# Optimization experiments

Hardware: AMD Instinct MI355X
Metric: run time of the kernel (lower is better)

Reference implementation:

```python
import jax, jax.numpy as jnp
import numpy as np

D = 1024
HS = 64
NH = D // HS


def setup_inputs() -> dict:
    key = jax.random.key(0)
    ks = jax.random.split(key, 8)
    B, S = 2, 2048
    x = jax.random.normal(ks[0], (B, S, D), dtype=jnp.float32)
    y = jax.random.normal(ks[1], (B, S, D), dtype=jnp.float32)
    pad_mask = jax.random.randint(ks[2], (B, S), 0, 2).astype(jnp.int32)
    sc = 1.0 / np.sqrt(D)
    Wq = jax.random.normal(ks[3], (D, D), dtype=jnp.float32) * sc
    Wk = jax.random.normal(ks[4], (D, D), dtype=jnp.float32) * sc
    Wv = jax.random.normal(ks[5], (D, D), dtype=jnp.float32) * sc
    Wp = jax.random.normal(ks[6], (D, D), dtype=jnp.float32) * sc
    bp = jnp.zeros((D,), dtype=jnp.float32)
    return {"x": x, "y": y, "pad_mask": pad_mask, "Wq": Wq, "Wk": Wk, "Wv": Wv, "Wp": Wp, "bp": bp}


def reference(x, y, pad_mask, Wq, Wk, Wv, Wp, bp):
    B, S, _ = x.shape
    # torch Linear: out = in @ W.T  (bias=False for q/k/v)
    q = (y @ Wq.T).reshape(B, S, NH, HS).transpose(0, 2, 1, 3)  # [B,H,S,hs]
    k = (x @ Wk.T).reshape(B, S, NH, HS).transpose(0, 2, 1, 3)
    v = (x @ Wv.T).reshape(B, S, NH, HS).transpose(0, 2, 1, 3)
    att = jnp.einsum('bhqd,bhkd->bhqk', q, k) * (HS ** -0.5)  # [B,H,S,S]
    att = jnp.where((pad_mask == 0)[:, None, None, :], -jnp.inf, att)
    att = jax.nn.softmax(att, axis=-1)
    out = jnp.einsum('bhqk,bhkd->bhqd', att, v)  # [B,H,S,hs]
    out = out.transpose(0, 2, 1, 3).reshape(B, S, D)
    return out @ Wp.T + bp
```

## Files before the change

### kernel.cpp

```cpp
#include <hip/hip_runtime.h>
#include <hip/hip_bf16.h>
#include <stdint.h>

typedef unsigned short u16;
typedef unsigned int u32;
typedef float __attribute__((ext_vector_type(4))) f32x4;
typedef __bf16 __attribute__((ext_vector_type(8))) bfrag;
typedef u16 __attribute__((ext_vector_type(8))) u16x8;

#define DEV static __device__ __forceinline__

DEV u16 f2bf(float f) {
  union { float f; u32 u; } c; c.f = f;
  u32 u = c.u;
  u += 0x7fffu + ((u >> 16) & 1u);
  return (u16)(u >> 16);
}

DEV u16 bf16bits(float f) {
  __hip_bfloat16 h = __float2bfloat16(f);
  return *reinterpret_cast<u16*>(&h);
}

typedef const u32 __attribute__((address_space(1)))* gas_t;
typedef u32 __attribute__((address_space(3)))* las_t;

DEV void async16(const void* g, void* l) {
  __builtin_amdgcn_global_load_lds((gas_t)(uintptr_t)g, (las_t)(uintptr_t)l, 16, 0, 0);
}

__global__ __launch_bounds__(256) void convert_all(
    const float* __restrict__ x, const float* __restrict__ y,
    const float* __restrict__ wq, const float* __restrict__ wk,
    const float* __restrict__ wv, const float* __restrict__ wp,
    u16* __restrict__ xb, u16* __restrict__ yb,
    u16* __restrict__ wqb, u16* __restrict__ wkb,
    u16* __restrict__ wvb, u16* __restrict__ wpb) {
  const int NX4 = (2 * 2048 * 1024) / 4;
  const int NW4 = (1024 * 1024) / 4;
  const int total = 2 * NX4 + 4 * NW4;
  for (int i = blockIdx.x * blockDim.x + threadIdx.x; i < total;
       i += gridDim.x * blockDim.x) {
    const float4* s; ushort4* d; int off;
    if (i < NX4) { s = (const float4*)x; d = (ushort4*)xb; off = i; }
    else if (i < 2 * NX4) { s = (const float4*)y; d = (ushort4*)yb; off = i - NX4; }
    else {
      int k = i - 2 * NX4; int wsel = k >> 18; off = k & (NW4 - 1);
      s = (const float4*)(wsel == 0 ? wq : wsel == 1 ? wk : wsel == 2 ? wv : wp);
      d = (ushort4*)(wsel == 0 ? wqb : wsel == 1 ? wkb : wsel == 2 ? wvb : wpb);
    }
    float4 v = s[off];
    ushort4 o; o.x = f2bf(v.x); o.y = f2bf(v.y); o.z = f2bf(v.z); o.w = f2bf(v.w);
    d[off] = o;
  }
}

__global__ __launch_bounds__(256, 3) void gemm_qkv(
    const u16* __restrict__ xb, const u16* __restrict__ yb,
    const u16* __restrict__ wqb, const u16* __restrict__ wkb,
    const u16* __restrict__ wvb,
    u16* __restrict__ Qb, u16* __restrict__ Kb2, u16* __restrict__ Vtb) {
  const int Kd = 1024, Nd = 1024;
  __shared__ __align__(16) u16 Als[128 * 32];
  __shared__ __align__(16) u16 Bls[128 * 32];
  __shared__ __align__(16) u16 Tls[4][64 * 72];

  const int gid = blockIdx.x;
  const int seg = gid >> 8;
  const int bb = gid & 255;
  const int m0 = (bb >> 3) * 128, n0 = (bb & 7) * 128;
  const u16* A  = (seg == 0) ? yb : xb;
  const u16* Bw = (seg == 0) ? wqb : (seg == 1 ? wkb : wvb);

  const int t = threadIdx.x;
  const int lane = t & 63, w = t >> 6;
  const int wr = w >> 1, wc = w & 1;
  const int r15 = lane & 15, g = lane >> 4;
  const int rs = t >> 2, sg = t & 3;

  f32x4 acc[4][4] = {{}};
  const u16* ga = A + (size_t)(m0 + rs) * Kd + sg * 8;
  const u16* gb = Bw + (size_t)(n0 + rs) * Kd + sg * 8;

  for (int k0 = 0; k0 < Kd; k0 += 32) {
    async16(ga + k0, &Als[t * 8]);
    async16(ga + 64 * Kd + k0, &Als[(t + 256) * 8]);
    async16(gb + k0, &Bls[t * 8]);
    async16(gb + 64 * Kd + k0, &Bls[(t + 256) * 8]);
    __syncthreads();
    bfrag af[4], bfr[4];
#pragma unroll
    for (int i = 0; i < 4; i++)
      af[i] = *(const bfrag*)&Als[(wr * 64 + i * 16 + r15) * 32 + g * 8];
#pragma unroll
    for (int i = 0; i < 4; i++)
      bfr[i] = *(const bfrag*)&Bls[(wc * 64 + i * 16 + r15) * 32 + g * 8];
#pragma unroll
    for (int i = 0; i < 4; i++)
#pragma unroll
      for (int j = 0; j < 4; j++)
        acc[i][j] = __builtin_amdgcn_mfma_f32_16x16x32_bf16(af[i], bfr[j], acc[i][j], 0, 0, 0);
    __syncthreads();
  }

  if (seg < 2) {
    u16* C = (seg == 0) ? Qb : Kb2;
    const float scale = (seg == 0) ? 0.125f : 1.0f;
#pragma unroll
    for (int i = 0; i < 4; i++) {
#pragma unroll
      for (int j = 0; j < 4; j++) {
        int col = n0 + wc * 64 + j * 16 + r15;
        int row = m0 + wr * 64 + i * 16 + g * 4;
#pragma unroll
        for (int r = 0; r < 4; r++)
          C[(size_t)(row + r) * Nd + col] = f2bf(acc[i][j][r] * scale);
      }
    }
  } else {
#pragma unroll
    for (int i = 0; i < 4; i++)
#pragma unroll
      for (int j = 0; j < 4; j++)
#pragma unroll
        for (int r = 0; r < 4; r++)
          Tls[w][(j * 16 + r15) * 72 + (i * 16 + g * 4 + r)] = f2bf(acc[i][j][r]);
#pragma unroll
    for (int it = 0; it < 8; ++it) {
      int slot = lane + it * 64;
      int nl = slot >> 3, sgm = slot & 7;
      int4 vrow = *(const int4*)&Tls[w][nl * 72 + sgm * 8];
      int col = n0 + wc * 64 + nl;
      int h = col >> 6, hs = col & 63;
      int rowg = m0 + wr * 64 + sgm * 8;
      int b = rowg >> 11, s = rowg & 2047;
      *(int4*)&Vtb[(((size_t)b * 16 + h) * 64 + hs) * 2048 + s] = vrow;
    }
  }
}

__global__ __launch_bounds__(256, 3) void gemm_proj(
    const u16* __restrict__ A, const u16* __restrict__ Bw,
    float* __restrict__ C, const float* __restrict__ bias) {
  const int Kd = 1024, Nd = 1024;
  __shared__ __align__(16) u16 Als[128 * 32];
  __shared__ __align__(16) u16 Bls[128 * 32];
  const int t = threadIdx.x;
  const int lane = t & 63, w = t >> 6;
  const int wr = w >> 1, wc = w & 1;
  const int r15 = lane & 15, g = lane >> 4;
  const int m0 = blockIdx.y * 128, n0 = blockIdx.x * 128;
  const int rs = t >> 2, sg = t & 3;

  f32x4 acc[4][4] = {{}};
  const u16* ga = A + (size_t)(m0 + rs) * Kd + sg * 8;
  const u16* gb = Bw + (size_t)(n0 + rs) * Kd + sg * 8;

  for (int k0 = 0; k0 < Kd; k0 += 32) {
    async16(ga + k0, &Als[t * 8]);
    async16(ga + 64 * Kd + k0, &Als[(t + 256) * 8]);
    async16(gb + k0, &Bls[t * 8]);
    async16(gb + 64 * Kd + k0, &Bls[(t + 256) * 8]);
    __syncthreads();
    bfrag af[4], bfr[4];
#pragma unroll
    for (int i = 0; i < 4; i++)
      af[i] = *(const bfrag*)&Als[(wr * 64 + i * 16 + r15) * 32 + g * 8];
#pragma unroll
    for (int i = 0; i < 4; i++)
      bfr[i] = *(const bfrag*)&Bls[(wc * 64 + i * 16 + r15) * 32 + g * 8];
#pragma unroll
    for (int i = 0; i < 4; i++)
#pragma unroll
      for (int j = 0; j < 4; j++)
        acc[i][j] = __builtin_amdgcn_mfma_f32_16x16x32_bf16(af[i], bfr[j], acc[i][j], 0, 0, 0);
    __syncthreads();
  }

#pragma unroll
  for (int i = 0; i < 4; i++) {
#pragma unroll
    for (int j = 0; j < 4; j++) {
      int col = n0 + wc * 64 + j * 16 + r15;
      int row = m0 + wr * 64 + i * 16 + g * 4;
      float bv = bias[col];
#pragma unroll
      for (int r = 0; r < 4; r++)
        C[(size_t)(row + r) * Nd + col] = acc[i][j][r] + bv;
    }
  }
}

__global__ __launch_bounds__(256, 2) void attn_fwd(
    const u16* __restrict__ Q, const u16* __restrict__ Kb,
    const u16* __restrict__ Vt, const int* __restrict__ mask,
    u16* __restrict__ O) {
  __shared__ __align__(16) u16 Kls[64 * 64];
  __shared__ __align__(16) u16 Vls[64 * 64];
  __shared__ __align__(16) u16 Pls[4][32 * 64];
  __shared__ float biasl[64];

  const int bid = blockIdx.x;
  const int swz = (bid & 7) * 64 + (bid >> 3);
  const int qblk = swz & 15, bh = swz >> 4;
  const int b = bh >> 4, h = bh & 15;
  const int t = threadIdx.x, lane = t & 63, w = t >> 6;
  const int r15 = lane & 15, g = lane >> 4;
  const int qbase = qblk * 128 + w * 32;

  bfrag aQ[2][2];
  {
    const u16* Qg = Q + ((size_t)b * 2048 + qbase) * 1024 + h * 64;
#pragma unroll
    for (int mf = 0; mf < 2; ++mf)
#pragma unroll
      for (int ks = 0; ks < 2; ++ks)
        aQ[mf][ks] = *(const bfrag*)&Qg[(size_t)(mf * 16 + r15) * 1024 + ks * 32 + g * 8];
  }

  bfrag ones;
  {
    u16x8 ob = {0x3F80, 0x3F80, 0x3F80, 0x3F80, 0x3F80, 0x3F80, 0x3F80, 0x3F80};
    ones = *(bfrag*)&ob;
  }

  f32x4 oacc[2][4] = {};
  f32x4 osum[2] = {};

  const u16* Kg = Kb + (size_t)b * 2048 * 1024 + h * 64;
  const u16* Vg = Vt + (size_t)bh * 64 * 2048;
  const int* mg = mask + b * 2048;

  const int kr = t >> 2, kc = (t & 3) * 16;
  const int swr = (kr & 7) << 3;
  const int rdx = (r15 & 7) << 3;
  int4 nk0, nk1, nv0, nv1; float nbias = 0.f;

  auto stage_load = [&](int kv0) {
    nk0 = *(const int4*)&Kg[(size_t)(kv0 + kr) * 1024 + kc];
    nk1 = *(const int4*)&Kg[(size_t)(kv0 + kr) * 1024 + kc + 8];
    nv0 = *(const int4*)&Vg[(size_t)kr * 2048 + kv0 + kc];
    nv1 = *(const int4*)&Vg[(size_t)kr * 2048 + kv0 + kc + 8];
    if (t < 64) nbias = mg[kv0 + t] ? 0.f : -1e30f;
  };
  auto stage_write = [&]() {
    *(int4*)&Kls[kr * 64 + (kc ^ swr)] = nk0;
    *(int4*)&Kls[kr * 64 + ((kc + 8) ^ swr)] = nk1;
    *(int4*)&Vls[kr * 64 + (kc ^ swr)] = nv0;
    *(int4*)&Vls[kr * 64 + ((kc + 8) ^ swr)] = nv1;
    if (t < 64) biasl[t] = nbias;
  };

  stage_load(0);
  stage_write();
  __syncthreads();

  for (int kt = 0; kt < 32; ++kt) {
    if (kt < 31) stage_load((kt + 1) * 64);

    f32x4 sc[2][4] = {};
#pragma unroll
    for (int ks = 0; ks < 2; ++ks) {
      const int cb = (ks * 32 + g * 8) ^ rdx;
#pragma unroll
      for (int nf = 0; nf < 4; ++nf) {
        bfrag bK = *(const bfrag*)&Kls[(nf * 16 + r15) * 64 + cb];
#pragma unroll
        for (int mf = 0; mf < 2; ++mf)
          sc[mf][nf] = __builtin_amdgcn_mfma_f32_16x16x32_bf16(aQ[mf][ks], bK, sc[mf][nf], 0, 0, 0);
      }
    }

    float bcol[4];
#pragma unroll
    for (int nf = 0; nf < 4; ++nf) bcol[nf] = biasl[nf * 16 + r15];

#pragma unroll
    for (int mf = 0; mf < 2; ++mf)
#pragma unroll
      for (int i = 0; i < 4; i++) {
        const int prow = mf * 16 + g * 4 + i;
        const int pxr = (prow & 7) << 3;
        u16* pr = &Pls[w][prow * 64];
#pragma unroll
        for (int nf = 0; nf < 4; ++nf) {
          float p = __expf(sc[mf][nf][i] + bcol[nf]);
          pr[(nf * 16 + r15) ^ pxr] = bf16bits(p);
        }
      }

#pragma unroll
    for (int ks = 0; ks < 2; ++ks) {
      const int cb = (ks * 32 + g * 8) ^ rdx;
      bfrag aP[2];
#pragma unroll
      for (int mf = 0; mf < 2; ++mf)
        aP[mf] = *(const bfrag*)&Pls[w][(mf * 16 + r15) * 64 + cb];
#pragma unroll
      for (int nf = 0; nf < 4; ++nf) {
        bfrag bV = *(const bfrag*)&Vls[(nf * 16 + r15) * 64 + cb];
#pragma unroll
        for (int mf = 0; mf < 2; ++mf)
          oacc[mf][nf] = __builtin_amdgcn_mfma_f32_16x16x32_bf16(aP[mf], bV, oacc[mf][nf], 0, 0, 0);
      }
#pragma unroll
      for (int mf = 0; mf < 2; ++mf)
        osum[mf] = __builtin_amdgcn_mfma_f32_16x16x32_bf16(aP[mf], ones, osum[mf], 0, 0, 0);
    }

    __syncthreads();
    if (kt < 31) {
      stage_write();
      __syncthreads();
    }
  }

  u16* Og = O + ((size_t)b * 2048 + qbase) * 1024 + h * 64;
#pragma unroll
  for (int mf = 0; mf < 2; ++mf)
#pragma unroll
    for (int i = 0; i < 4; i++) {
      float rl = 1.f / osum[mf][i];
      size_t ro = (size_t)(mf * 16 + g * 4 + i) * 1024;
#pragma unroll
      for (int nf = 0; nf < 4; ++nf)
        Og[ro + nf * 16 + r15] = f2bf(oacc[mf][nf][i] * rl);
    }
}

extern "C" void kernel_launch(void* const* d_in, const int* in_sizes, int n_in,
                              void* d_out, int out_size, void* d_ws, size_t ws_size,
                              hipStream_t stream) {
  const float* x  = (const float*)d_in[0];
  const float* y  = (const float*)d_in[1];
  const int*  msk = (const int*)d_in[2];
  const float* Wq = (const float*)d_in[3];
  const float* Wk = (const float*)d_in[4];
  const float* Wv = (const float*)d_in[5];
  const float* Wp = (const float*)d_in[6];
  const float* bp = (const float*)d_in[7];

  char* ws = (char*)d_ws;
  const size_t SZ_XB = (size_t)2 * 2048 * 1024 * 2;
  const size_t SZ_W  = (size_t)1024 * 1024 * 2;
  u16* xb  = (u16*)(ws);
  u16* yb  = (u16*)(ws + SZ_XB);
  u16* wqb = (u16*)(ws + 2 * SZ_XB);
  u16* wkb = (u16*)(ws + 2 * SZ_XB + SZ_W);
  u16* wvb = (u16*)(ws + 2 * SZ_XB + 2 * SZ_W);
  u16* wpb = (u16*)(ws + 2 * SZ_XB + 3 * SZ_W);
  u16* Qb  = (u16*)(ws + 2 * SZ_XB + 4 * SZ_W);
  u16* Kb2 = (u16*)(ws + 3 * SZ_XB + 4 * SZ_W);
  u16* Vtb = (u16*)(ws + 4 * SZ_XB + 4 * SZ_W);
  u16* Ob  = (u16*)(ws + 5 * SZ_XB + 4 * SZ_W);

  convert_all<<<2048, 256, 0, stream>>>(x, y, Wq, Wk, Wv, Wp, xb, yb, wqb, wkb, wvb, wpb);
  gemm_qkv<<<768, 256, 0, stream>>>(xb, yb, wqb, wkb, wvb, Qb, Kb2, Vtb);
  attn_fwd<<<512, 256, 0, stream>>>(Qb, Kb2, Vtb, msk, Ob);
  dim3 gg(8, 32);
  gemm_proj<<<gg, 256, 0, stream>>>(Ob, wpb, (float*)d_out, bp);
}
```

Measured before the change: 135.7 us.

## Double-buffer K/V tiles in attention with async global-to-LDS copies

Result: no change. 136.6 us (+0.7%).

```diff
diff --git a/kernel.cpp b/kernel.cpp
--- a/kernel.cpp
+++ b/kernel.cpp
@@ -195,10 +195,10 @@
     const u16* __restrict__ Q, const u16* __restrict__ Kb,
     const u16* __restrict__ Vt, const int* __restrict__ mask,
     u16* __restrict__ O) {
-  __shared__ __align__(16) u16 Kls[64 * 64];
-  __shared__ __align__(16) u16 Vls[64 * 64];
+  __shared__ __align__(16) u16 Kls[2][64 * 64];
+  __shared__ __align__(16) u16 Vls[2][64 * 64];
   __shared__ __align__(16) u16 Pls[4][32 * 64];
-  __shared__ float biasl[64];
+  __shared__ float biasl[2][64];
 
   const int bid = blockIdx.x;
   const int swz = (bid & 7) * 64 + (bid >> 3);
@@ -231,32 +231,29 @@
   const u16* Vg = Vt + (size_t)bh * 64 * 2048;
   const int* mg = mask + b * 2048;
 
-  const int kr = t >> 2, kc = (t & 3) * 16;
-  const int swr = (kr & 7) << 3;
   const int rdx = (r15 & 7) << 3;
-  int4 nk0, nk1, nv0, nv1; float nbias = 0.f;
-
-  auto stage_load = [&](int kv0) {
-    nk0 = *(const int4*)&Kg[(size_t)(kv0 + kr) * 1024 + kc];
-    nk1 = *(const int4*)&Kg[(size_t)(kv0 + kr) * 1024 + kc + 8];
-    nv0 = *(const int4*)&Vg[(size_t)kr * 2048 + kv0 + kc];
-    nv1 = *(const int4*)&Vg[(size_t)kr * 2048 + kv0 + kc + 8];
-    if (t < 64) nbias = mg[kv0 + t] ? 0.f : -1e30f;
+
+  const int srow = t >> 3;
+  const int scol = (((t & 7) ^ (srow & 7)) * 8);
+
+  auto stage_async = [&](int kv0, int buf) {
+    async16(&Kg[(size_t)(kv0 + srow) * 1024 + scol],        &Kls[buf][t * 8]);
+    async16(&Kg[(size_t)(kv0 + 32 + srow) * 1024 + scol],   &Kls[buf][2048 + t * 8]);
+    async16(&Vg[(size_t)srow * 2048 + kv0 + scol],          &Vls[buf][t * 8]);
+    async16(&Vg[(size_t)(32 + srow) * 2048 + kv0 + scol],   &Vls[buf][2048 + t * 8]);
   };
-  auto stage_write = [&]() {
-    *(int4*)&Kls[kr * 64 + (kc ^ swr)] = nk0;
-    *(int4*)&Kls[kr * 64 + ((kc + 8) ^ swr)] = nk1;
-    *(int4*)&Vls[kr * 64 + (kc ^ swr)] = nv0;
-    *(int4*)&Vls[kr * 64 + ((kc + 8) ^ swr)] = nv1;
-    if (t < 64) biasl[t] = nbias;
-  };
-
-  stage_load(0);
-  stage_write();
+
+  stage_async(0, 0);
+  if (t < 64) biasl[0][t] = mg[t] ? 0.f : -1e30f;
   __syncthreads();
 
+  float nbias = 0.f;
   for (int kt = 0; kt < 32; ++kt) {
-    if (kt < 31) stage_load((kt + 1) * 64);
+    const int cur = kt & 1;
+    if (kt < 31) {
+      stage_async((kt + 1) * 64, cur ^ 1);
+      if (t < 64) nbias = mg[(kt + 1) * 64 + t] ? 0.f : -1e30f;
+    }
 
     f32x4 sc[2][4] = {};
 #pragma unroll
@@ -264,7 +261,7 @@
       const int cb = (ks * 32 + g * 8) ^ rdx;
 #pragma unroll
       for (int nf = 0; nf < 4; ++nf) {
-        bfrag bK = *(const bfrag*)&Kls[(nf * 16 + r15) * 64 + cb];
+        bfrag bK = *(const bfrag*)&Kls[cur][(nf * 16 + r15) * 64 + cb];
 #pragma unroll
         for (int mf = 0; mf < 2; ++mf)
           sc[mf][nf] = __builtin_amdgcn_mfma_f32_16x16x32_bf16(aQ[mf][ks], bK, sc[mf][nf], 0, 0, 0);
@@ -273,7 +270,7 @@
 
     float bcol[4];
 #pragma unroll
-    for (int nf = 0; nf < 4; ++nf) bcol[nf] = biasl[nf * 16 + r15];
+    for (int nf = 0; nf < 4; ++nf) bcol[nf] = biasl[cur][nf * 16 + r15];
 
 #pragma unroll
     for (int mf = 0; mf < 2; ++mf)
@@ -298,7 +295,7 @@
         aP[mf] = *(const bfrag*)&Pls[w][(mf * 16 + r15) * 64 + cb];
 #pragma unroll
       for (int nf = 0; nf < 4; ++nf) {
-        bfrag bV = *(const bfrag*)&Vls[(nf * 16 + r15) * 64 + cb];
+        bfrag bV = *(const bfrag*)&Vls[cur][(nf * 16 + r15) * 64 + cb];
 #pragma unroll
         for (int mf = 0; mf < 2; ++mf)
           oacc[mf][nf] = __builtin_amdgcn_mfma_f32_16x16x32_bf16(aP[mf], bV, oacc[mf][nf], 0, 0, 0);
@@ -308,11 +305,8 @@
         osum[mf] = __builtin_amdgcn_mfma_f32_16x16x32_bf16(aP[mf], ones, osum[mf], 0, 0, 0);
     }
 
-    __syncthreads();
-    if (kt < 31) {
-      stage_write();
-      __syncthreads();
-    }
+    if (kt < 31 && t < 64) biasl[cur ^ 1][t] = nbias;
+    __syncthreads();
   }
 
   u16* Og = O + ((size_t)b * 2048 + qbase) * 1024 + h * 64;
```
